# Optimization experiments

Hardware: AMD Instinct MI355X
Metric: run time of the kernel (lower is better)

The kernel has to match this reference:

```python
import jax, jax.numpy as jnp
import numpy as np

# Config (lite version of KimiK2): 2 layers, dim 2048, 16 heads x 128, MLA latent rank 512,
# 4 experts / top-2, SwiGLU inter dim 1024, vocab 32000, batch 2, seq 1024.
DEPTH, DIM, H, HD, R, DFF, E, TOPK, V, B, S = 2, 2048, 16, 128, 512, 1024, 4, 2, 32000, 2, 1024
EPS = 1e-6


def rmsnorm(x, w):
    var = jnp.mean(jnp.square(x), axis=-1, keepdims=True)
    return x * jax.lax.rsqrt(var + EPS) * w


def setup_inputs() -> dict:
    key = jax.random.key(0)
    ks = jax.random.split(key, 16)
    sd = 0.02
    d = {
        'x_tokens': jax.random.randint(ks[0], (B, S), 0, V),
        'emb': jax.random.normal(ks[1], (V, DIM), jnp.float32) * sd,
        'embed_norm_w': jnp.ones((DIM,), jnp.float32),
        # per-layer stacked params (leading axis DEPTH)
        'norm_w': jnp.ones((DEPTH, DIM), jnp.float32),
        'Wq': jax.random.normal(ks[2], (DEPTH, DIM, H * HD), jnp.float32) * sd,
        'Wdkv': jax.random.normal(ks[3], (DEPTH, DIM, R), jnp.float32) * sd,
        'Wuk': jax.random.normal(ks[4], (DEPTH, R, H * HD), jnp.float32) * sd,
        'Wuv': jax.random.normal(ks[5], (DEPTH, R, H * HD), jnp.float32) * sd,
        'Wo': jax.random.normal(ks[6], (DEPTH, H * HD, DIM), jnp.float32) * sd,
        'Wg': jax.random.normal(ks[7], (DEPTH, DIM, E), jnp.float32) * sd,
        'W1': jax.random.normal(ks[8], (DEPTH, E, DIM, DFF), jnp.float32) * sd,
        'W3': jax.random.normal(ks[9], (DEPTH, E, DIM, DFF), jnp.float32) * sd,
        'W2': jax.random.normal(ks[10], (DEPTH, E, DFF, DIM), jnp.float32) * sd,
        'head_norm_w': jnp.ones((DIM,), jnp.float32),
        'head_W': jax.random.normal(ks[11], (DIM, V), jnp.float32) * sd,
        'head_b': jnp.zeros((V,), jnp.float32),
    }
    return d


def mla(x, Wq, Wdkv, Wuk, Wuv, Wo):
    # Multi-head latent attention: queries from x, K/V from a low-rank latent c.
    Bq, Sq, _ = x.shape
    q = (x @ Wq).reshape(Bq, Sq, H, HD)
    c = x @ Wdkv                                   # [B,S,R] compressed KV latent
    k = (c @ Wuk).reshape(Bq, Sq, H, HD)
    v = (c @ Wuv).reshape(Bq, Sq, H, HD)
    scores = jnp.einsum('bqhd,bkhd->bhqk', q, k) / jnp.sqrt(jnp.float32(HD))
    a = jax.nn.softmax(scores, axis=-1)            # block never passes a mask -> full attention
    o = jnp.einsum('bhqk,bkhd->bqhd', a, v).reshape(Bq, Sq, H * HD)
    return o @ Wo


def moe(x, Wg, W1, W3, W2):
    # x: [B,S,D] -> flatten tokens. Dense-over-experts (E=4) with top-k masked gates.
    Bq, Sq, Dq = x.shape
    xt = x.reshape(Bq * Sq, Dq)                    # [T,D]
    gate = jax.nn.softmax(xt @ Wg, axis=-1)        # [T,E]
    topv, topi = jax.lax.top_k(gate, TOPK)
    topv = topv / jnp.sum(topv, axis=-1, keepdims=True)
    gw = jnp.zeros_like(gate).at[jnp.arange(xt.shape[0])[:, None], topi].set(topv)  # [T,E]
    h = jnp.einsum('td,edf->etf', xt, W1)
    g = jnp.einsum('td,edf->etf', xt, W3)
    eo = jnp.einsum('etf,efd->etd', jax.nn.silu(h) * g, W2)
    out = jnp.einsum('etd,te->td', eo, gw)
    return out.reshape(Bq, Sq, Dq)


def reference(x_tokens, emb, embed_norm_w, norm_w, Wq, Wdkv, Wuk, Wuv, Wo, Wg, W1, W3, W2, head_norm_w, head_W, head_b):
    h = emb[x_tokens]
    h = rmsnorm(h, embed_norm_w)

    def layer(h, p):
        nw, wq, wdkv, wuk, wuv, wo, wg, w1, w3, w2 = p
        h = h + mla(rmsnorm(h, nw), wq, wdkv, wuk, wuv, wo)
        # NOTE: same norm weight reused pre-MoE, as in the torch module
        h = h + moe(rmsnorm(h, nw), wg, w1, w3, w2)
        return h, None

    h, _ = jax.lax.scan(layer, h, (norm_w, Wq, Wdkv, Wuk, Wuv, Wo, Wg, W1, W3, W2))
    return rmsnorm(h, head_norm_w) @ head_W + head_b
```

## Files before the change

kernel.cpp:

```cpp
#include <hip/hip_runtime.h>
#include <hip/hip_bf16.h>

typedef __hip_bfloat16 bf16;
typedef __bf16 bf16x8 __attribute__((ext_vector_type(8)));
typedef float f32x4 __attribute__((ext_vector_type(4)));
typedef unsigned short u16;
typedef unsigned int u32;
typedef __attribute__((address_space(1))) const void* gptr_t;
typedef __attribute__((address_space(3))) void* lptr_t;

static constexpr int TOKS = 2048, DM = 2048, RL = 512, DF = 1024, SQ = 1024, NV = 32000;
static constexpr int CAP = 1536;
static constexpr long PL_X  = (long)TOKS * DM;
static constexpr long PL_C  = (long)TOKS * RL;
static constexpr long PL_VT = 2l * 16 * 128 * 1024;
static constexpr long M4 = 4l * 1024 * 1024;
static constexpr long M2 = 2l * 1024 * 1024;

__device__ __forceinline__ float b2f(bf16 x){ return __bfloat162float(x); }
__device__ __forceinline__ bf16  f2b(float x){ return __float2bfloat16(x); }
__device__ __forceinline__ void split1(float x, u16& h, u16& l){
  bf16 hb = f2b(x);
  float r = x - b2f(hb);
  bf16 lb = f2b(r);
  h = *(u16*)&hb; l = *(u16*)&lb;
}

__device__ __forceinline__ float block_red(float v, int op){
  __shared__ float red[4];
  const int lane = threadIdx.x & 63, wv = threadIdx.x >> 6;
  #pragma unroll
  for (int off = 32; off > 0; off >>= 1){
    float o = __shfl_down(v, off, 64);
    v = op ? fmaxf(v, o) : v + o;
  }
  __syncthreads();
  if (lane == 0) red[wv] = v;
  __syncthreads();
  float r = red[0];
  #pragma unroll
  for (int i = 1; i < 4; ++i) r = op ? fmaxf(r, red[i]) : r + red[i];
  return r;
}

__global__ __launch_bounds__(256)
void embed_norm_k(const int* __restrict__ toks, const float* __restrict__ emb,
                  const float* __restrict__ w, float* __restrict__ h){
  const int t = blockIdx.x;
  const long tok = toks[t];
  const int base = threadIdx.x * 8;
  const float* ep = emb + tok * (long)DM + base;
  float4 va = *(const float4*)ep, vb = *(const float4*)(ep + 4);
  float v[8] = {va.x, va.y, va.z, va.w, vb.x, vb.y, vb.z, vb.w};
  float ss = 0.f;
  #pragma unroll
  for (int i = 0; i < 8; ++i) ss += v[i]*v[i];
  ss = block_red(ss, 0);
  const float inv = rsqrtf(ss / DM + 1e-6f);
  float4 wa = *(const float4*)(w + base), wb4 = *(const float4*)(w + base + 4);
  float wv[8] = {wa.x, wa.y, wa.z, wa.w, wb4.x, wb4.y, wb4.z, wb4.w};
  float* hp = h + (long)t * DM + base;
  #pragma unroll
  for (int i = 0; i < 8; ++i) hp[i] = v[i] * inv * wv[i];
}

__global__ __launch_bounds__(256)
void rmsnorm_planes_k(const float* __restrict__ h, const float* __restrict__ w,
                      u16* __restrict__ hi, u16* __restrict__ lo){
  const int t = blockIdx.x;
  const int base = threadIdx.x * 8;
  const float* hp = h + (long)t * DM + base;
  float4 va = *(const float4*)hp, vb = *(const float4*)(hp + 4);
  float v[8] = {va.x, va.y, va.z, va.w, vb.x, vb.y, vb.z, vb.w};
  float ss = 0.f;
  #pragma unroll
  for (int i = 0; i < 8; ++i) ss += v[i]*v[i];
  ss = block_red(ss, 0);
  const float inv = rsqrtf(ss / DM + 1e-6f);
  float4 wa = *(const float4*)(w + base), wb4 = *(const float4*)(w + base + 4);
  float wv[8] = {wa.x, wa.y, wa.z, wa.w, wb4.x, wb4.y, wb4.z, wb4.w};
  u16 hvv[8], lvv[8];
  #pragma unroll
  for (int i = 0; i < 8; ++i) split1(v[i] * inv * wv[i], hvv[i], lvv[i]);
  *(int4*)(hi + (long)t * DM + base) = *(const int4*)hvv;
  *(int4*)(lo + (long)t * DM + base) = *(const int4*)lvv;
}

__global__ __launch_bounds__(256)
void gate_k(const float* __restrict__ h, const float* __restrict__ nw,
            const float* __restrict__ Wg, float* __restrict__ gw){
  const int t = blockIdx.x;
  const int base = threadIdx.x * 8;
  const float* hp = h + (long)t * DM + base;
  float4 va = *(const float4*)hp, vb = *(const float4*)(hp + 4);
  float v[8] = {va.x, va.y, va.z, va.w, vb.x, vb.y, vb.z, vb.w};
  float ss = 0.f;
  #pragma unroll
  for (int i = 0; i < 8; ++i) ss += v[i]*v[i];
  ss = block_red(ss, 0);
  const float inv = rsqrtf(ss / DM + 1e-6f);
  float a[4] = {0.f, 0.f, 0.f, 0.f};
  #pragma unroll
  for (int i = 0; i < 8; ++i){
    const float xv = v[i] * inv * nw[base + i];
    #pragma unroll
    for (int e = 0; e < 4; ++e) a[e] += xv * Wg[(base + i)*4 + e];
  }
  #pragma unroll
  for (int e = 0; e < 4; ++e) a[e] = block_red(a[e], 0);
  if (threadIdx.x == 0){
    int i1 = 0;
    for (int e = 1; e < 4; ++e) if (a[e] > a[i1]) i1 = e;
    int i2 = -1;
    for (int e = 0; e < 4; ++e){ if (e == i1) continue; if (i2 < 0 || a[e] > a[i2]) i2 = e; }
    float g[4];
    const float m = fmaxf(fmaxf(a[0], a[1]), fmaxf(a[2], a[3]));
    float s = 0.f;
    for (int e = 0; e < 4; ++e){ g[e] = __expf(a[e] - m); s += g[e]; }
    for (int e = 0; e < 4; ++e) g[e] /= s;
    const float ns = g[i1] + g[i2];
    float* op = gw + (long)t * 4;
    op[0] = 0.f; op[1] = 0.f; op[2] = 0.f; op[3] = 0.f;
    op[i1] = g[i1] / ns; op[i2] = g[i2] / ns;
  }
}

__global__ __launch_bounds__(256)
void build_lists_k(const float* __restrict__ gw, int* __restrict__ idx, int* __restrict__ cnt){
  const int e = threadIdx.x >> 6, lane = threadIdx.x & 63;
  int base = 0;
  for (int t0 = 0; t0 < TOKS; t0 += 64){
    const int t = t0 + lane;
    const bool sel = gw[(long)t * 4 + e] > 0.f;
    const unsigned long long m = __ballot(sel);
    const int pos = __popcll(m & ((1ull << lane) - 1ull));
    if (sel && base + pos < CAP) idx[e * CAP + base + pos] = t;
    base += (int)__popcll(m);
  }
  if (lane == 0) cnt[e] = base < CAP ? base : CAP;
}

__global__ __launch_bounds__(256)
void gather2_k(const u16* __restrict__ xph, const int* __restrict__ idx,
               const int* __restrict__ cnt, int ebase, u16* __restrict__ xg){
  const int e = blockIdx.x / CAP, r = blockIdx.x % CAP;
  if (r >= cnt[ebase + e]) return;
  const long t = idx[(long)(ebase + e) * CAP + r];
  const int c = threadIdx.x * 8;
  const long dst = ((long)e * 2 * CAP + r) * DM + c;
  *(int4*)(xg + dst) = *(const int4*)(xph + t * DM + c);
  *(int4*)(xg + dst + (long)CAP * DM) = *(const int4*)(xph + PL_X + t * DM + c);
}

__global__ __launch_bounds__(256)
void gatherb_k(const u16* __restrict__ xph, const int* __restrict__ idx,
               const int* __restrict__ cnt, u16* __restrict__ xgb){
  const int e = blockIdx.x / CAP, r = blockIdx.x % CAP;
  if (r >= cnt[e]) return;
  const long t = idx[(long)e * CAP + r];
  const int c = threadIdx.x * 8;
  *(int4*)(xgb + ((long)e * CAP + r) * DM + c) = *(const int4*)(xph + t * DM + c);
}

__global__ __launch_bounds__(256)
void softmax_pack_k(float* __restrict__ pf){
  const long row = blockIdx.x;
  const float* pr = pf + row * SQ;
  const int base = threadIdx.x * 4;
  float4 v4 = *(const float4*)(pr + base);
  float v[4] = {v4.x, v4.y, v4.z, v4.w};
  float m = fmaxf(fmaxf(v[0], v[1]), fmaxf(v[2], v[3]));
  m = block_red(m, 1);
  float s = 0.f;
  #pragma unroll
  for (int i = 0; i < 4; ++i){ v[i] = __expf(v[i] - m); s += v[i]; }
  s = block_red(s, 0);
  const float inv = 1.f / s;
  u16 hv[4], lv[4];
  #pragma unroll
  for (int i = 0; i < 4; ++i) split1(v[i] * inv, hv[i], lv[i]);
  u16* out = (u16*)pf + row * 2048;
  *(int2*)(out + base) = *(const int2*)hv;
  *(int2*)(out + 1024 + base) = *(const int2*)lv;
}

__global__ __launch_bounds__(256)
void swiglu_pack_k(float* __restrict__ h1, const float* __restrict__ h3){
  const int t = threadIdx.x;
  const long r = (long)blockIdx.x * 2 + (t >> 7);
  const int col = (t & 127) * 8;
  const float* p1 = h1 + r * 1024 + col;
  const float* p3 = h3 + r * 1024 + col;
  float4 a0 = *(const float4*)p1, a1 = *(const float4*)(p1 + 4);
  float4 b0 = *(const float4*)p3, b1 = *(const float4*)(p3 + 4);
  float a[8] = {a0.x, a0.y, a0.z, a0.w, a1.x, a1.y, a1.z, a1.w};
  float b[8] = {b0.x, b0.y, b0.z, b0.w, b1.x, b1.y, b1.z, b1.w};
  u16 hv[8], lv[8];
  #pragma unroll
  for (int j = 0; j < 8; ++j){
    const float y = (a[j] / (1.f + __expf(-a[j]))) * b[j];
    split1(y, hv[j], lv[j]);
  }
  __syncthreads();
  u16* out = (u16*)h1 + r * 2048;
  *(int4*)(out + col) = *(const int4*)hv;
  *(int4*)(out + 1024 + col) = *(const int4*)lv;
}

__global__ __launch_bounds__(256)
void swiglu_bk(bf16* __restrict__ h1, const bf16* __restrict__ h3){
  const long i = ((long)blockIdx.x * 256 + threadIdx.x) * 8;
  union { int4 i4; bf16 b[8]; } x, y;
  x.i4 = *(const int4*)(h1 + i);
  y.i4 = *(const int4*)(h3 + i);
  #pragma unroll
  for (int j = 0; j < 8; ++j){
    const float a = b2f(x.b[j]);
    const float b = b2f(y.b[j]);
    x.b[j] = f2b((a / (1.f + __expf(-a))) * b);
  }
  *(int4*)(h1 + i) = x.i4;
}

__global__ __launch_bounds__(256)
void tsplit_k(const float* __restrict__ in, long inz, int ldin,
              u16* __restrict__ oh, u16* __restrict__ ol, long outz, int ldout, int ntx){
  __shared__ u16 lh[64][72], ll[64][72];
  const int z = blockIdx.z;
  in += (long)z * inz; oh += (long)z * outz; ol += (long)z * outz;
  const int bx = blockIdx.x % ntx, by = blockIdx.x / ntx;
  const int k0 = by * 64, n0 = bx * 64;
  const int t = threadIdx.x;
  {
    const int r = t >> 2, cb = (t & 3) * 16;
    const float* ip = in + (long)(k0 + r) * ldin + n0 + cb;
    #pragma unroll
    for (int i = 0; i < 16; i += 4){
      float4 v = *(const float4*)(ip + i);
      float a[4] = {v.x, v.y, v.z, v.w};
      #pragma unroll
      for (int j = 0; j < 4; ++j){
        u16 hv, lv; split1(a[j], hv, lv);
        lh[r][cb + i + j] = hv; ll[r][cb + i + j] = lv;
      }
    }
  }
  __syncthreads();
  {
    const int n = t >> 2, kb = (t & 3) * 16;
    u16 hv[16], lv[16];
    #pragma unroll
    for (int i = 0; i < 16; ++i){ hv[i] = lh[kb + i][n]; lv[i] = ll[kb + i][n]; }
    u16* po = oh + (long)(n0 + n) * ldout + k0 + kb;
    u16* pl = ol + (long)(n0 + n) * ldout + k0 + kb;
    *(int4*)po = *(const int4*)hv; *(int4*)(po + 8) = *(const int4*)(hv + 8);
    *(int4*)pl = *(const int4*)lv; *(int4*)(pl + 8) = *(const int4*)(lv + 8);
  }
}

__global__ __launch_bounds__(256)
void tconv_k(const float* __restrict__ in, long inz, int ldin,
             bf16* __restrict__ out, long outz, int ldout, int ntx){
  __shared__ u16 lh[64][72];
  const int z = blockIdx.z;
  in += (long)z * inz; out += (long)z * outz;
  const int bx = blockIdx.x % ntx, by = blockIdx.x / ntx;
  const int k0 = by * 64, n0 = bx * 64;
  const int t = threadIdx.x;
  {
    const int r = t >> 2, cb = (t & 3) * 16;
    const float* ip = in + (long)(k0 + r) * ldin + n0 + cb;
    #pragma unroll
    for (int i = 0; i < 16; i += 4){
      float4 v = *(const float4*)(ip + i);
      float a[4] = {v.x, v.y, v.z, v.w};
      #pragma unroll
      for (int j = 0; j < 4; ++j){ bf16 hb = f2b(a[j]); lh[r][cb + i + j] = *(u16*)&hb; }
    }
  }
  __syncthreads();
  {
    const int n = t >> 2, kb = (t & 3) * 16;
    u16 hv[16];
    #pragma unroll
    for (int i = 0; i < 16; ++i) hv[i] = lh[kb + i][n];
    u16* po = (u16*)out + (long)(n0 + n) * ldout + k0 + kb;
    *(int4*)po = *(const int4*)hv; *(int4*)(po + 8) = *(const int4*)(hv + 8);
  }
}

__device__ __forceinline__ int swz64(int r, int c){
  return ((((c >> 3) + r) & 7) << 3) | (c & 7);
}
__device__ __forceinline__ int2 tile_xy(int ny){
  const int nwg = gridDim.x;
  const int wid = blockIdx.x;
  const int q = nwg >> 3, r = nwg & 7;
  const int xcd = wid & 7, pos = wid >> 3;
  const int lid = (xcd < r) ? (xcd*(q+1) + pos) : (r*(q+1) + (xcd - r)*q + pos);
  return make_int2(lid / ny, lid % ny);
}

__device__ __forceinline__ void stage64(const u16* src, int ld, int rbase, int k0,
                                        u16* lp, int sub, int lane){
  const int r = sub * 8 + (lane >> 3);
  const int cs = ((lane & 7) - r) & 7;
  const u16* g = src + (long)(rbase + r) * ld + k0 + cs * 8;
  __builtin_amdgcn_global_load_lds((gptr_t)g, (lptr_t)(lp + sub * 512), 16, 0, 0);
}

template<int MT, int OM>
__global__ __launch_bounds__(256)
void gemms_nt(const u16* __restrict__ Ah, const u16* __restrict__ Al, long ab, int lda,
              const u16* __restrict__ Bh, const u16* __restrict__ Bl, long bb, int ldb,
              void* __restrict__ Cv, long cb, int ldc, long cpl,
              int K, float scale, const float* __restrict__ aux, int gst, int ny,
              const int* __restrict__ rowmap, const int* __restrict__ cntp)
{
  __shared__ __align__(16) u16 ash[MT*32][64], asl[MT*32][64];
  __shared__ __align__(16) u16 bsh[128][64], bsl[128][64];
  const int z = blockIdx.z;
  Ah += (long)z * ab; Al += (long)z * ab;
  Bh += (long)z * bb; Bl += (long)z * bb;
  const int2 tt = tile_xy(ny);
  const int m0 = tt.y * (MT*32), n0 = tt.x * 128;
  int cntv = 1 << 30;
  if (cntp){ cntv = cntp[z]; if (m0 >= cntv) return; }
  const int tid = threadIdx.x, lane = tid & 63, wv = tid >> 6;
  const int wr = (wv >> 1) * (MT*16), wc = (wv & 1) * 64;
  const int fr = lane & 15, fk = (lane >> 4) * 8;

  f32x4 acc[MT][4] = {};
  constexpr int AI4 = MT * 4;

  for (int k0 = 0; k0 < K; k0 += 64){
    __syncthreads();
    #pragma unroll
    for (int ii = 0; ii < 2*AI4 + 32; ++ii){
      if ((ii & 3) != wv) continue;
      if (ii < AI4)             stage64(Ah, lda, m0, k0, &ash[0][0], ii, lane);
      else if (ii < 2*AI4)      stage64(Al, lda, m0, k0, &asl[0][0], ii - AI4, lane);
      else if (ii < 2*AI4 + 16) stage64(Bh, ldb, n0, k0, &bsh[0][0], ii - 2*AI4, lane);
      else                      stage64(Bl, ldb, n0, k0, &bsl[0][0], ii - 2*AI4 - 16, lane);
    }
    __syncthreads();
    bf16x8 ahf[MT][2], alf[MT][2], bhf[4][2], blf[4][2];
    #pragma unroll
    for (int mi = 0; mi < MT; ++mi){
      const int rr = wr + mi * 16 + fr;
      #pragma unroll
      for (int ks = 0; ks < 2; ++ks){
        const int sc = swz64(rr, ks * 32 + fk);
        ahf[mi][ks] = *(const bf16x8*)&ash[rr][sc];
        alf[mi][ks] = *(const bf16x8*)&asl[rr][sc];
      }
    }
    #pragma unroll
    for (int ni = 0; ni < 4; ++ni){
      const int rr = wc + ni * 16 + fr;
      #pragma unroll
      for (int ks = 0; ks < 2; ++ks){
        const int sc = swz64(rr, ks * 32 + fk);
        bhf[ni][ks] = *(const bf16x8*)&bsh[rr][sc];
        blf[ni][ks] = *(const bf16x8*)&bsl[rr][sc];
      }
    }
    #pragma unroll
    for (int mi = 0; mi < MT; ++mi)
      #pragma unroll
      for (int ni = 0; ni < 4; ++ni)
        #pragma unroll
        for (int ks = 0; ks < 2; ++ks){
          acc[mi][ni] = __builtin_amdgcn_mfma_f32_16x16x32_bf16(ahf[mi][ks], bhf[ni][ks], acc[mi][ni], 0, 0, 0);
          acc[mi][ni] = __builtin_amdgcn_mfma_f32_16x16x32_bf16(ahf[mi][ks], blf[ni][ks], acc[mi][ni], 0, 0, 0);
          acc[mi][ni] = __builtin_amdgcn_mfma_f32_16x16x32_bf16(alf[mi][ks], bhf[ni][ks], acc[mi][ni], 0, 0, 0);
        }
  }

  const int crow = (lane >> 4) * 4, ccol = lane & 15;
  #pragma unroll
  for (int mi = 0; mi < MT; ++mi){
    #pragma unroll
    for (int ni = 0; ni < 4; ++ni){
      const int gm0 = m0 + wr + mi * 16 + crow;
      const int gn = n0 + wc + ni * 16 + ccol;
      if (OM == 5){
        u16 hv[4], lv[4];
        #pragma unroll
        for (int j = 0; j < 4; ++j) split1(acc[mi][ni][j], hv[j], lv[j]);
        const long off = (((long)(gm0 >> 10) * 16 + (gn >> 7)) * 128 + (gn & 127)) * 1024 + (gm0 & 1023);
        u16* vt = (u16*)Cv;
        *(int2*)(vt + off) = *(const int2*)hv;
        *(int2*)(vt + cpl + off) = *(const int2*)lv;
      } else if (OM == 6){
        #pragma unroll
        for (int j = 0; j < 4; ++j){
          const int row = gm0 + j;
          if (row < cntv){
            const long t = rowmap[(long)z * CAP + row];
            ((float*)Cv)[t * ldc + gn] += aux[t * gst] * acc[mi][ni][j];
          }
        }
      } else {
        #pragma unroll
        for (int j = 0; j < 4; ++j){
          const long off = (long)z * cb + (long)(gm0 + j) * ldc + gn;
          const float v = acc[mi][ni][j];
          if (OM == 0)      ((float*)Cv)[off] = v * scale;
          else if (OM == 1) ((float*)Cv)[off] += v;
          else if (OM == 3) ((float*)Cv)[off] += aux[(long)(gm0 + j) * gst] * v;
          else { u16 hv, lv; split1(v, hv, lv); ((u16*)Cv)[off] = hv; ((u16*)Cv)[off + cpl] = lv; }
        }
      }
    }
  }
}

template<int MT, int OM>
__global__ __launch_bounds__(256)
void gemmb_nt(const bf16* __restrict__ A, long ab, int lda,
              const bf16* __restrict__ B, long bb, int ldb,
              void* __restrict__ Cv, long cb, int ldc,
              int K, const float* __restrict__ aux, int gst, int ny,
              const int* __restrict__ rowmap, const int* __restrict__ cntp)
{
  __shared__ __align__(16) u16 a_lds[MT*32][64];
  __shared__ __align__(16) u16 b_lds[128][64];
  const int z = blockIdx.z;
  A += (long)z * ab; B += (long)z * bb;
  const int2 tt = tile_xy(ny);
  const int m0 = tt.y * (MT*32), n0 = tt.x * 128;
  int cntv = 1 << 30;
  if (cntp){ cntv = cntp[z]; if (m0 >= cntv) return; }
  const int tid = threadIdx.x, lane = tid & 63, wv = tid >> 6;
  const int wr = (wv >> 1) * (MT*16), wc = (wv & 1) * 64;
  const int fr = lane & 15, fk = (lane >> 4) * 8;

  f32x4 acc[MT][4] = {};
  constexpr int AI4 = MT * 4;

  for (int k0 = 0; k0 < K; k0 += 64){
    __syncthreads();
    #pragma unroll
    for (int ii = 0; ii < AI4 + 16; ++ii){
      if ((ii & 3) != wv) continue;
      if (ii < AI4) stage64((const u16*)A, lda, m0, k0, &a_lds[0][0], ii, lane);
      else          stage64((const u16*)B, ldb, n0, k0, &b_lds[0][0], ii - AI4, lane);
    }
    __syncthreads();
    bf16x8 af[MT][2], bfv[4][2];
    #pragma unroll
    for (int mi = 0; mi < MT; ++mi){
      const int rr = wr + mi * 16 + fr;
      #pragma unroll
      for (int ks = 0; ks < 2; ++ks)
        af[mi][ks] = *(const bf16x8*)&a_lds[rr][swz64(rr, ks * 32 + fk)];
    }
    #pragma unroll
    for (int ni = 0; ni < 4; ++ni){
      const int rr = wc + ni * 16 + fr;
      #pragma unroll
      for (int ks = 0; ks < 2; ++ks)
        bfv[ni][ks] = *(const bf16x8*)&b_lds[rr][swz64(rr, ks * 32 + fk)];
    }
    #pragma unroll
    for (int mi = 0; mi < MT; ++mi)
      #pragma unroll
      for (int ni = 0; ni < 4; ++ni)
        #pragma unroll
        for (int ks = 0; ks < 2; ++ks)
          acc[mi][ni] = __builtin_amdgcn_mfma_f32_16x16x32_bf16(af[mi][ks], bfv[ni][ks], acc[mi][ni], 0, 0, 0);
  }

  const int crow = (lane >> 4) * 4, ccol = lane & 15;
  #pragma unroll
  for (int mi = 0; mi < MT; ++mi){
    #pragma unroll
    for (int ni = 0; ni < 4; ++ni){
      const int gm0 = m0 + wr + mi * 16 + crow;
      const int gn = n0 + wc + ni * 16 + ccol;
      #pragma unroll
      for (int j = 0; j < 4; ++j){
        const float v = acc[mi][ni][j];
        if (OM == 7){
          const int row = gm0 + j;
          if (row < cntv){
            const long t = rowmap[(long)z * CAP + row];
            atomicAdd(&((float*)Cv)[t * ldc + gn], aux[t * gst + z] * v);
          }
        } else {
          const long off = (long)z * cb + (long)(gm0 + j) * ldc + gn;
          if (OM == 0)      ((bf16*)Cv)[off] = f2b(v);
          else if (OM == 2) ((float*)Cv)[off] = v + aux[gn];
          else              atomicAdd(&((float*)Cv)[off], aux[(long)(gm0 + j) * gst + z] * v);
        }
      }
    }
  }
}

extern "C" void kernel_launch(void* const* d_in, const int* in_sizes, int n_in,
                              void* d_out, int out_size, void* d_ws, size_t ws_size,
                              hipStream_t stream)
{
  (void)in_sizes; (void)n_in; (void)out_size; (void)ws_size;
  const int*   toks = (const int*)d_in[0];
  const float* emb  = (const float*)d_in[1];
  const float* enw  = (const float*)d_in[2];
  const float* nw   = (const float*)d_in[3];
  const float* Wq   = (const float*)d_in[4];
  const float* Wdkv = (const float*)d_in[5];
  const float* Wuk  = (const float*)d_in[6];
  const float* Wuv  = (const float*)d_in[7];
  const float* Wo   = (const float*)d_in[8];
  const float* Wg   = (const float*)d_in[9];
  const float* W1   = (const float*)d_in[10];
  const float* W3   = (const float*)d_in[11];
  const float* W2   = (const float*)d_in[12];
  const float* hnw  = (const float*)d_in[13];
  const float* hW   = (const float*)d_in[14];
  const float* hb   = (const float*)d_in[15];

  const size_t MB = 1ull << 20;
  char* ws = (char*)d_ws;
  float* h    = (float*)(ws);
  float* gw   = (float*)(ws + 16*MB);
  int*   idx  = (int*)(ws + 16*MB + 128*1024);
  int*   cnt  = (int*)(ws + 16*MB + 256*1024);
  u16*   xph  = (u16*)(ws + 17*MB);
  u16*   wpl  = (u16*)(ws + 33*MB);
  u16*   qph  = (u16*)(ws + 49*MB);
  u16*   cph  = (u16*)(ws + 65*MB);
  u16*   kph  = (u16*)(ws + 69*MB);
  u16*   vtp  = (u16*)(ws + 85*MB);
  u16*   oph  = (u16*)(ws + 101*MB);
  float* pf   = (float*)(ws + 17*MB);
  u16*   xg   = (u16*)(ws + 49*MB);
  float* h1f  = (float*)(ws + 73*MB);
  float* h3f  = (float*)(ws + 85*MB);
  bf16*  wT   = (bf16*)(ws + 33*MB);
  u16*   xgb  = (u16*)(ws + 49*MB);
  bf16*  h1b  = (bf16*)(ws + 73*MB);
  bf16*  h3b  = (bf16*)(ws + 85*MB);
  bf16*  whT  = (bf16*)(ws + 33*MB);

  const float qscale = 0.08838834764831845f;

  embed_norm_k<<<TOKS, 256, 0, stream>>>(toks, emb, enw, h);

  for (int l = 0; l < 2; ++l){
    const float* nwl = nw + (long)l * DM;
    rmsnorm_planes_k<<<TOKS, 256, 0, stream>>>(h, nwl, xph, xph + PL_X);

    tsplit_k<<<1024, 256, 0, stream>>>(Wq + (long)l*DM*DM, 0, DM, wpl, wpl + M4, 0, DM, 32);
    gemms_nt<2,4><<<dim3(512,1,1), 256, 0, stream>>>(xph, xph + PL_X, 0, DM, wpl, wpl + M4, 0, DM,
        qph, 0, DM, PL_X, DM, 1.f, nullptr, 0, 32, nullptr, nullptr);
    tsplit_k<<<256, 256, 0, stream>>>(Wdkv + (long)l*DM*RL, 0, RL, wpl, wpl + M2, 0, DM, 8);
    gemms_nt<2,4><<<dim3(128,1,1), 256, 0, stream>>>(xph, xph + PL_X, 0, DM, wpl, wpl + M2, 0, DM,
        cph, 0, RL, PL_C, DM, 1.f, nullptr, 0, 32, nullptr, nullptr);
    tsplit_k<<<256, 256, 0, stream>>>(Wuk + (long)l*RL*DM, 0, DM, wpl, wpl + M2, 0, RL, 32);
    gemms_nt<2,4><<<dim3(512,1,1), 256, 0, stream>>>(cph, cph + PL_C, 0, RL, wpl, wpl + M2, 0, RL,
        kph, 0, DM, PL_X, RL, 1.f, nullptr, 0, 32, nullptr, nullptr);
    tsplit_k<<<256, 256, 0, stream>>>(Wuv + (long)l*RL*DM, 0, DM, wpl, wpl + M2, 0, RL, 32);
    gemms_nt<2,5><<<dim3(512,1,1), 256, 0, stream>>>(cph, cph + PL_C, 0, RL, wpl, wpl + M2, 0, RL,
        vtp, 0, 0, PL_VT, RL, 1.f, nullptr, 0, 32, nullptr, nullptr);

    for (int b = 0; b < 2; ++b){
      for (int hg = 0; hg < 2; ++hg){
        const long qo = (long)b*SQ*DM + hg*1024;
        gemms_nt<4,0><<<dim3(64,1,8), 256, 0, stream>>>(qph + qo, qph + PL_X + qo, 128, DM,
            kph + qo, kph + PL_X + qo, 128, DM,
            pf, (long)SQ*SQ, SQ, 0, 128, qscale, nullptr, 0, 8, nullptr, nullptr);
        softmax_pack_k<<<8*SQ, 256, 0, stream>>>(pf);
        const long vo = ((long)b*16 + hg*8) * 128 * 1024;
        gemms_nt<1,4><<<dim3(32,1,8), 256, 0, stream>>>((const u16*)pf, (const u16*)pf + 1024,
            1024l*2048, 2048,
            vtp + vo, vtp + PL_VT + vo, 128l*1024, 1024,
            oph + (long)b*SQ*DM + hg*1024, 128, DM, PL_X, SQ, 1.f, nullptr, 0, 32, nullptr, nullptr);
      }
    }

    tsplit_k<<<1024, 256, 0, stream>>>(Wo + (long)l*DM*DM, 0, DM, wpl, wpl + M4, 0, DM, 32);
    gemms_nt<2,1><<<dim3(512,1,1), 256, 0, stream>>>(oph, oph + PL_X, 0, DM, wpl, wpl + M4, 0, DM,
        h, 0, DM, 0, DM, 1.f, nullptr, 0, 32, nullptr, nullptr);

    gate_k<<<TOKS, 256, 0, stream>>>(h, nwl, Wg + (long)l*DM*4, gw);
    build_lists_k<<<1, 256, 0, stream>>>(gw, idx, cnt);
    rmsnorm_planes_k<<<TOKS, 256, 0, stream>>>(h, nwl, xph, xph + PL_X);

    if (l == 0){
      for (int p2 = 0; p2 < 2; ++p2){
        const int ebase = p2 * 2;
        const long wo13 = ((long)l*4 + ebase) * (long)DM * DF;
        gather2_k<<<2*CAP, 256, 0, stream>>>(xph, idx, cnt, ebase, xg);
        tsplit_k<<<dim3(512,1,2), 256, 0, stream>>>(W1 + wo13, (long)DM*DF, DF, wpl, wpl + M4, M2, DM, 16);
        gemms_nt<2,0><<<dim3(192,1,2), 256, 0, stream>>>(xg, xg + (long)CAP*DM, 2l*CAP*DM, DM,
            wpl, wpl + M4, M2, DM, h1f, (long)CAP*DF, DF, 0, DM, 1.f, nullptr, 0, 24,
            nullptr, cnt + ebase);
        tsplit_k<<<dim3(512,1,2), 256, 0, stream>>>(W3 + wo13, (long)DM*DF, DF, wpl, wpl + M4, M2, DM, 16);
        gemms_nt<2,0><<<dim3(192,1,2), 256, 0, stream>>>(xg, xg + (long)CAP*DM, 2l*CAP*DM, DM,
            wpl, wpl + M4, M2, DM, h3f, (long)CAP*DF, DF, 0, DM, 1.f, nullptr, 0, 24,
            nullptr, cnt + ebase);
        swiglu_pack_k<<<CAP, 256, 0, stream>>>(h1f, h3f);
        tsplit_k<<<dim3(512,1,2), 256, 0, stream>>>(W2 + ((long)l*4 + ebase)*(long)DF*DM, (long)DF*DM, DM,
            wpl, wpl + M4, M2, DF, 32);
        for (int ei = 0; ei < 2; ++ei){
          gemms_nt<2,6><<<dim3(384,1,1), 256, 0, stream>>>(
              (const u16*)h1f + (long)ei*CAP*2048, (const u16*)h1f + (long)ei*CAP*2048 + 1024,
              0, 2048, wpl + (long)ei*M2, wpl + M4 + (long)ei*M2, 0, DF,
              h, 0, DM, 0, DF, 1.f, gw + ebase + ei, 4, 24,
              idx + (ebase + ei)*CAP, cnt + ebase + ei);
        }
      }
    } else {
      gatherb_k<<<4*CAP, 256, 0, stream>>>(xph, idx, cnt, xgb);
      tconv_k<<<dim3(512,1,4), 256, 0, stream>>>(W1 + (long)l*4*DM*DF, (long)DM*DF, DF, wT, M2, DM, 16);
      gemmb_nt<2,0><<<dim3(192,1,4), 256, 0, stream>>>((const bf16*)xgb, (long)CAP*DM, DM, wT, M2, DM,
          h1b, (long)CAP*DF, DF, DM, nullptr, 0, 24, nullptr, cnt);
      tconv_k<<<dim3(512,1,4), 256, 0, stream>>>(W3 + (long)l*4*DM*DF, (long)DM*DF, DF, wT, M2, DM, 16);
      gemmb_nt<2,0><<<dim3(192,1,4), 256, 0, stream>>>((const bf16*)xgb, (long)CAP*DM, DM, wT, M2, DM,
          h3b, (long)CAP*DF, DF, DM, nullptr, 0, 24, nullptr, cnt);
      swiglu_bk<<<(4*CAP*DF)/2048, 256, 0, stream>>>(h1b, h3b);
      tconv_k<<<dim3(512,1,4), 256, 0, stream>>>(W2 + (long)l*4*DF*DM, (long)DF*DM, DM, wT, M2, DF, 32);
      gemmb_nt<2,7><<<dim3(384,1,4), 256, 0, stream>>>(h1b, (long)CAP*DF, DF, wT, M2, DF,
          h, 0, DM, DF, gw, 4, 24, idx, cnt);
    }
  }

  rmsnorm_planes_k<<<TOKS, 256, 0, stream>>>(h, hnw, xph, xph + PL_X);
  for (int half = 0; half < 2; ++half){
    tconv_k<<<8000, 256, 0, stream>>>(hW + half*16000, 0, NV, whT, 0, DM, 250);
    gemmb_nt<4,2><<<dim3(2000,1,1), 256, 0, stream>>>((const bf16*)xph, 0, DM, whT, 0, DM,
        (float*)d_out + half*16000, 0, NV, DM, hb + half*16000, 0, 16, nullptr, nullptr);
  }
}
```

Baseline: 2.196 ms.

## Replace bf16 GEMM with double-buffered 128x256 tile kernel using async LDS loads

Replaces the single-buffered bf16 GEMM with a new kernel that uses 128x256 output tiles, K-step 32, and two LDS buffers. The next K-slice is prefetched via global_load_lds while the current one is consumed, gated by explicit vmcnt waits and raw barriers. Larger tiles raise data reuse per block and the double buffering is meant to hide global-load latency. The trade-offs are higher register pressure (128 accumulators per thread), fewer blocks per grid, and wasted padded columns on the vocab head, where a column bound check handles the 16000-wide halves.

After: 2.678 ms. +21.9%, slower.

```diff
diff --git a/kernel.cpp b/kernel.cpp
--- a/kernel.cpp
+++ b/kernel.cpp
@@ -292,6 +292,9 @@
 __device__ __forceinline__ int swz64(int r, int c){
   return ((((c >> 3) + r) & 7) << 3) | (c & 7);
 }
+__device__ __forceinline__ int swz2(int r, int c){
+  return ((((c >> 3) + (r >> 1)) & 3) << 3) | (c & 7);
+}
 __device__ __forceinline__ int2 tile_xy(int ny){
   const int nwg = gridDim.x;
   const int wid = blockIdx.x;
@@ -307,6 +310,26 @@
   const int cs = ((lane & 7) - r) & 7;
   const u16* g = src + (long)(rbase + r) * ld + k0 + cs * 8;
   __builtin_amdgcn_global_load_lds((gptr_t)g, (lptr_t)(lp + sub * 512), 16, 0, 0);
+}
+__device__ __forceinline__ void stage32(const u16* src, int ld, int rbase, int k0,
+                                        u16* lp, int sub, int lane){
+  const int r = sub * 16 + (lane >> 2);
+  const int cs = ((lane & 3) - (r >> 1)) & 3;
+  const u16* g = src + (long)(rbase + r) * ld + k0 + cs * 8;
+  __builtin_amdgcn_global_load_lds((gptr_t)g, (lptr_t)(lp + sub * 512), 16, 0, 0);
+}
+
+template<int N> __device__ __forceinline__ void wait_vmcnt(){
+  if constexpr (N == 0) asm volatile("s_waitcnt vmcnt(0)" ::: "memory");
+  else if constexpr (N == 6) asm volatile("s_waitcnt vmcnt(6)" ::: "memory");
+  __builtin_amdgcn_sched_barrier(0);
+}
+__device__ __forceinline__ void barrier_raw(){
+  __builtin_amdgcn_sched_barrier(0);
+  asm volatile("" ::: "memory");
+  __builtin_amdgcn_s_barrier();
+  asm volatile("" ::: "memory");
+  __builtin_amdgcn_sched_barrier(0);
 }
 
 template<int MT, int OM>
@@ -416,68 +439,73 @@
   }
 }
 
-template<int MT, int OM>
-__global__ __launch_bounds__(256)
-void gemmb_nt(const bf16* __restrict__ A, long ab, int lda,
+template<int OM>
+__global__ __launch_bounds__(256)
+void gemmw_nt(const bf16* __restrict__ A, long ab, int lda,
               const bf16* __restrict__ B, long bb, int ldb,
               void* __restrict__ Cv, long cb, int ldc,
-              int K, const float* __restrict__ aux, int gst, int ny,
+              int K, const float* __restrict__ aux, int gst, int ny, int nlim,
               const int* __restrict__ rowmap, const int* __restrict__ cntp)
 {
-  __shared__ __align__(16) u16 a_lds[MT*32][64];
-  __shared__ __align__(16) u16 b_lds[128][64];
+  __shared__ __align__(16) u16 a_lds[2][128][32];
+  __shared__ __align__(16) u16 b_lds[2][256][32];
   const int z = blockIdx.z;
   A += (long)z * ab; B += (long)z * bb;
   const int2 tt = tile_xy(ny);
-  const int m0 = tt.y * (MT*32), n0 = tt.x * 128;
+  const int m0 = tt.y * 128, n0 = tt.x * 256;
   int cntv = 1 << 30;
   if (cntp){ cntv = cntp[z]; if (m0 >= cntv) return; }
   const int tid = threadIdx.x, lane = tid & 63, wv = tid >> 6;
-  const int wr = (wv >> 1) * (MT*16), wc = (wv & 1) * 64;
+  const int wc = wv * 64;
   const int fr = lane & 15, fk = (lane >> 4) * 8;
 
-  f32x4 acc[MT][4] = {};
-  constexpr int AI4 = MT * 4;
-
-  for (int k0 = 0; k0 < K; k0 += 64){
-    __syncthreads();
-    #pragma unroll
-    for (int ii = 0; ii < AI4 + 16; ++ii){
+  f32x4 acc[8][4] = {};
+
+  auto STAGE = [&](int bf, int k0){
+    #pragma unroll
+    for (int ii = 0; ii < 24; ++ii){
       if ((ii & 3) != wv) continue;
-      if (ii < AI4) stage64((const u16*)A, lda, m0, k0, &a_lds[0][0], ii, lane);
-      else          stage64((const u16*)B, ldb, n0, k0, &b_lds[0][0], ii - AI4, lane);
-    }
-    __syncthreads();
-    bf16x8 af[MT][2], bfv[4][2];
-    #pragma unroll
-    for (int mi = 0; mi < MT; ++mi){
-      const int rr = wr + mi * 16 + fr;
-      #pragma unroll
-      for (int ks = 0; ks < 2; ++ks)
-        af[mi][ks] = *(const bf16x8*)&a_lds[rr][swz64(rr, ks * 32 + fk)];
-    }
+      if (ii < 8) stage32((const u16*)A, lda, m0, k0, &a_lds[bf][0][0], ii, lane);
+      else        stage32((const u16*)B, ldb, n0, k0, &b_lds[bf][0][0], ii - 8, lane);
+    }
+  };
+
+  STAGE(0, 0);
+  int cur = 0;
+  for (int k0 = 0; k0 < K; k0 += 32){
+    if (k0 + 32 < K){ STAGE(cur ^ 1, k0 + 32); wait_vmcnt<6>(); }
+    else              wait_vmcnt<0>();
+    barrier_raw();
+    bf16x8 bfv[4];
     #pragma unroll
     for (int ni = 0; ni < 4; ++ni){
       const int rr = wc + ni * 16 + fr;
-      #pragma unroll
-      for (int ks = 0; ks < 2; ++ks)
-        bfv[ni][ks] = *(const bf16x8*)&b_lds[rr][swz64(rr, ks * 32 + fk)];
-    }
-    #pragma unroll
-    for (int mi = 0; mi < MT; ++mi)
-      #pragma unroll
-      for (int ni = 0; ni < 4; ++ni)
+      bfv[ni] = *(const bf16x8*)&b_lds[cur][rr][swz2(rr, fk)];
+    }
+    #pragma unroll
+    for (int mih = 0; mih < 2; ++mih){
+      bf16x8 af[4];
+      #pragma unroll
+      for (int mj = 0; mj < 4; ++mj){
+        const int rr = mih * 64 + mj * 16 + fr;
+        af[mj] = *(const bf16x8*)&a_lds[cur][rr][swz2(rr, fk)];
+      }
+      #pragma unroll
+      for (int mj = 0; mj < 4; ++mj)
         #pragma unroll
-        for (int ks = 0; ks < 2; ++ks)
-          acc[mi][ni] = __builtin_amdgcn_mfma_f32_16x16x32_bf16(af[mi][ks], bfv[ni][ks], acc[mi][ni], 0, 0, 0);
+        for (int ni = 0; ni < 4; ++ni)
+          acc[mih*4 + mj][ni] = __builtin_amdgcn_mfma_f32_16x16x32_bf16(af[mj], bfv[ni], acc[mih*4 + mj][ni], 0, 0, 0);
+    }
+    barrier_raw();
+    cur ^= 1;
   }
 
   const int crow = (lane >> 4) * 4, ccol = lane & 15;
   #pragma unroll
-  for (int mi = 0; mi < MT; ++mi){
+  for (int mi = 0; mi < 8; ++mi){
     #pragma unroll
     for (int ni = 0; ni < 4; ++ni){
-      const int gm0 = m0 + wr + mi * 16 + crow;
+      const int gm0 = m0 + mi * 16 + crow;
       const int gn = n0 + wc + ni * 16 + ccol;
       #pragma unroll
       for (int j = 0; j < 4; ++j){
@@ -488,11 +516,14 @@
             const long t = rowmap[(long)z * CAP + row];
             atomicAdd(&((float*)Cv)[t * ldc + gn], aux[t * gst + z] * v);
           }
+        } else if (OM == 2){
+          if (gn < nlim){
+            const long off = (long)z * cb + (long)(gm0 + j) * ldc + gn;
+            ((float*)Cv)[off] = v + aux[gn];
+          }
         } else {
           const long off = (long)z * cb + (long)(gm0 + j) * ldc + gn;
-          if (OM == 0)      ((bf16*)Cv)[off] = f2b(v);
-          else if (OM == 2) ((float*)Cv)[off] = v + aux[gn];
-          else              atomicAdd(&((float*)Cv)[off], aux[(long)(gm0 + j) * gst + z] * v);
+          ((bf16*)Cv)[off] = f2b(v);
         }
       }
     }
@@ -615,22 +646,22 @@
     } else {
       gatherb_k<<<4*CAP, 256, 0, stream>>>(xph, idx, cnt, xgb);
       tconv_k<<<dim3(512,1,4), 256, 0, stream>>>(W1 + (long)l*4*DM*DF, (long)DM*DF, DF, wT, M2, DM, 16);
-      gemmb_nt<2,0><<<dim3(192,1,4), 256, 0, stream>>>((const bf16*)xgb, (long)CAP*DM, DM, wT, M2, DM,
-          h1b, (long)CAP*DF, DF, DM, nullptr, 0, 24, nullptr, cnt);
+      gemmw_nt<0><<<dim3(48,1,4), 256, 0, stream>>>((const bf16*)xgb, (long)CAP*DM, DM, wT, M2, DM,
+          h1b, (long)CAP*DF, DF, DM, nullptr, 0, 12, 1<<30, nullptr, cnt);
       tconv_k<<<dim3(512,1,4), 256, 0, stream>>>(W3 + (long)l*4*DM*DF, (long)DM*DF, DF, wT, M2, DM, 16);
-      gemmb_nt<2,0><<<dim3(192,1,4), 256, 0, stream>>>((const bf16*)xgb, (long)CAP*DM, DM, wT, M2, DM,
-          h3b, (long)CAP*DF, DF, DM, nullptr, 0, 24, nullptr, cnt);
+      gemmw_nt<0><<<dim3(48,1,4), 256, 0, stream>>>((const bf16*)xgb, (long)CAP*DM, DM, wT, M2, DM,
+          h3b, (long)CAP*DF, DF, DM, nullptr, 0, 12, 1<<30, nullptr, cnt);
       swiglu_bk<<<(4*CAP*DF)/2048, 256, 0, stream>>>(h1b, h3b);
       tconv_k<<<dim3(512,1,4), 256, 0, stream>>>(W2 + (long)l*4*DF*DM, (long)DF*DM, DM, wT, M2, DF, 32);
-      gemmb_nt<2,7><<<dim3(384,1,4), 256, 0, stream>>>(h1b, (long)CAP*DF, DF, wT, M2, DF,
-          h, 0, DM, DF, gw, 4, 24, idx, cnt);
+      gemmw_nt<7><<<dim3(96,1,4), 256, 0, stream>>>(h1b, (long)CAP*DF, DF, wT, M2, DF,
+          h, 0, DM, DF, gw, 4, 12, 1<<30, idx, cnt);
     }
   }
 
   rmsnorm_planes_k<<<TOKS, 256, 0, stream>>>(h, hnw, xph, xph + PL_X);
   for (int half = 0; half < 2; ++half){
     tconv_k<<<8000, 256, 0, stream>>>(hW + half*16000, 0, NV, whT, 0, DM, 250);
-    gemmb_nt<4,2><<<dim3(2000,1,1), 256, 0, stream>>>((const bf16*)xph, 0, DM, whT, 0, DM,
-        (float*)d_out + half*16000, 0, NV, DM, hb + half*16000, 0, 16, nullptr, nullptr);
-  }
-}
+    gemmw_nt<2><<<dim3(1008,1,1), 256, 0, stream>>>((const bf16*)xph, 0, DM, whT, 0, DM,
+        (float*)d_out + half*16000, 0, NV, DM, hb + half*16000, 0, 16, 16000, nullptr, nullptr);
+  }
+}
```
